# Kernel tuning notes

Measured on AMD Instinct MI355X. Metric: run time of the kernel, lower is better.

Reference implementation:

```python
import jax, jax.numpy as jnp
import numpy as np

B, S, D_MODEL, H_DIM = 8, 4096, 512, 120  # h = 1, so d_k = h_dim = 120
NEG_INF = jnp.float32(-1e9)
L2_EPS = 1e-12  # F.normalize eps


def setup_inputs() -> dict:
    key = jax.random.key(0)
    k_q, k_m, k_w, k_wt = jax.random.split(key, 4)
    query = jax.random.normal(k_q, (B, S, D_MODEL), dtype=jnp.float32)
    mask = jax.random.randint(k_m, (B, S, S), 0, 2, dtype=jnp.int32)
    # q_linear params (kaiming-uniform-ish init scale)
    lim = 1.0 / np.sqrt(D_MODEL)
    w_q = jax.random.uniform(k_w, (H_DIM, D_MODEL), jnp.float32, -lim, lim)
    b_q = jnp.zeros((H_DIM,), jnp.float32)
    # weight_tensor: shape (h, d_k) = (1, 120), xavier-uniform scale
    wt_lim = np.sqrt(6.0 / (1 + H_DIM))
    weight_tensor = jax.random.uniform(k_wt, (1, H_DIM), jnp.float32, -wt_lim, wt_lim)
    return {"query": query, "mask": mask, "w_q": w_q, "b_q": b_q,
            "weight_tensor": weight_tensor}


def reference(query, mask, w_q, b_q, weight_tensor):
    # context = q_linear(query).view(B, -1, h_dim); with h=1 the view is identity
    context = jnp.einsum("bsd,kd->bsk", query, w_q) + b_q          # [B, S, 120]
    # weighted then L2-normalized (cosine-similarity) features
    ctx = context * weight_tensor[:, None, :]                        # bcast (1,1,120)
    norm = jnp.sqrt(jnp.sum(ctx * ctx, axis=-1, keepdims=True))
    ctx_n = ctx / jnp.maximum(norm, L2_EPS)
    scores = jnp.einsum("bqk,bpk->bqp", ctx_n, ctx_n)               # [B, S, S]
    scores = jnp.where(mask == 0, NEG_INF, scores)                   # masked_fill
    return jax.nn.softmax(scores, axis=-1)                           # dropout: eval/identity
```

## Files before the change

### kernel.cpp

```cpp
#include <hip/hip_runtime.h>
#include <hip/hip_bf16.h>
#include <stdint.h>

#define BATCH 8
#define SEQ   4096
#define DM    512
#define HD    120

typedef __bf16   v8bf  __attribute__((ext_vector_type(8)));
typedef float    v4f   __attribute__((ext_vector_type(4)));
typedef int      i4    __attribute__((ext_vector_type(4)));
typedef uint32_t u32x2 __attribute__((ext_vector_type(2)));
typedef uint32_t u32x4 __attribute__((ext_vector_type(4)));
typedef float    f32x4 __attribute__((ext_vector_type(4)));

static __device__ __forceinline__ ushort f2bf(float x) {
  uint32_t u = __builtin_bit_cast(uint32_t, x);
  return (ushort)((u + 0x7fffu + ((u >> 16) & 1u)) >> 16);
}

static __device__ __forceinline__ void gld16(const void* g, void* l) {
  __builtin_amdgcn_global_load_lds(
      (const __attribute__((address_space(1))) uint32_t*)g,
      (__attribute__((address_space(3))) uint32_t*)l, 16, 0, 0);
}

__global__ __launch_bounds__(256) void ctx_kernel(
    const float* __restrict__ q, const float* __restrict__ wq,
    const float* __restrict__ bq, const float* __restrict__ wt,
    ushort* __restrict__ ctx)
{
  __shared__ __align__(16) float qs[32][68];
  __shared__ __align__(16) float ws2[32][136];

  const int t  = threadIdx.x;
  const int tx = t & 31, ty = t >> 5;
  const size_t row0 = (size_t)blockIdx.x * 64;
  const int qr = t >> 2, qk = (t & 3) * 8;

  float acc[8][4];
  #pragma unroll
  for (int j = 0; j < 8; ++j)
    #pragma unroll
    for (int i = 0; i < 4; ++i) acc[j][i] = 0.f;

  for (int k0 = 0; k0 < DM; k0 += 32) {
    __syncthreads();
    {
      f32x4 v0 = *(const f32x4*)&q[(row0 + qr) * DM + k0 + qk];
      f32x4 v1 = *(const f32x4*)&q[(row0 + qr) * DM + k0 + qk + 4];
      #pragma unroll
      for (int i = 0; i < 4; ++i) qs[qk + i][qr] = v0[i];
      #pragma unroll
      for (int i = 0; i < 4; ++i) qs[qk + 4 + i][qr] = v1[i];
    }
    #pragma unroll
    for (int i = 0; i < 16; ++i) {
      int flat = t + i * 256;
      int kk = flat & 31, c = flat >> 5;
      ws2[kk][c] = (c < HD) ? wq[c * DM + k0 + kk] : 0.f;
    }
    __syncthreads();
    #pragma unroll
    for (int kk = 0; kk < 32; ++kk) {
      f32x4 bv = *(const f32x4*)&ws2[kk][tx * 4];
      f32x4 a0 = *(const f32x4*)&qs[kk][ty * 8];
      f32x4 a1 = *(const f32x4*)&qs[kk][ty * 8 + 4];
      #pragma unroll
      for (int r = 0; r < 4; ++r)
        #pragma unroll
        for (int c = 0; c < 4; ++c) {
          acc[r][c]     = fmaf(a0[r], bv[c], acc[r][c]);
          acc[4 + r][c] = fmaf(a1[r], bv[c], acc[4 + r][c]);
        }
    }
  }

  float wtv[4], bqv[4];
  #pragma unroll
  for (int i = 0; i < 4; ++i) {
    int c = tx * 4 + i;
    wtv[i] = (c < HD) ? wt[c] : 0.f;
    bqv[i] = (c < HD) ? bq[c] : 0.f;
  }
  #pragma unroll
  for (int j = 0; j < 8; ++j) {
    int r = ty * 8 + j;
    float v[4]; float ss = 0.f;
    #pragma unroll
    for (int i = 0; i < 4; ++i) {
      v[i] = (acc[j][i] + bqv[i]) * wtv[i];
      ss = fmaf(v[i], v[i], ss);
    }
    #pragma unroll
    for (int xm = 1; xm < 32; xm <<= 1) ss += __shfl_xor(ss, xm, 64);
    float rinv = 1.f / fmaxf(sqrtf(ss), 1e-12f);
    uint32_t p0 = (uint32_t)f2bf(v[0] * rinv) | ((uint32_t)f2bf(v[1] * rinv) << 16);
    uint32_t p1 = (uint32_t)f2bf(v[2] * rinv) | ((uint32_t)f2bf(v[3] * rinv) << 16);
    u32x2 o = {p0, p1};
    char* dst = (char*)ctx + (row0 + r) * 256 +
                (((tx >> 1) * 16) ^ ((r & 7) << 4)) + (tx & 1) * 8;
    *(u32x2*)dst = o;
  }
}

#define MFMA(A, B, C) __builtin_amdgcn_mfma_f32_16x16x32_bf16(A, B, C, 0, 0, 0)

static __device__ __forceinline__ v8bf ldfrag(const char* base, int row, int slot) {
  int byte = row * 256 + ((slot * 16) ^ ((row & 7) << 4));
  return __builtin_bit_cast(v8bf, *(const u32x4*)(base + byte));
}

#define STAGE(buf, j) do {                                                    \
  const char* _gs = ctxb + (size_t)(j) * 64 * 256;                            \
  _Pragma("unroll")                                                           \
  for (int _i = 0; _i < 4; ++_i)                                              \
    gld16(_gs + (w * 4 + _i) * 1024 + lane * 16, (buf) + (w * 4 + _i) * 1024);\
} while (0)

#define LDM(dst, j) do {                                                      \
  _Pragma("unroll")                                                           \
  for (int _t = 0; _t < 4; ++_t)                                              \
    dst[_t] = *(const i4*)(mrow + (size_t)(j) * 64 + _t * 16 + g * 4);        \
} while (0)

#define QKT(buf, acc) do {                                                    \
  _Pragma("unroll")                                                           \
  for (int _t = 0; _t < 4; ++_t) {                                            \
    acc[_t] = (v4f){0.f, 0.f, 0.f, 0.f};                                      \
    _Pragma("unroll")                                                         \
    for (int _k = 0; _k < 4; ++_k) {                                          \
      v8bf _a = ldfrag(buf, _t * 16 + ln, _k * 4 + g);                        \
      acc[_t] = MFMA(_a, qf[_k], acc[_t]);                                    \
    }                                                                         \
  }                                                                           \
} while (0)

__global__ __launch_bounds__(256) void attn_kernel(
    const ushort* __restrict__ ctx, const int* __restrict__ mask,
    uint32_t* __restrict__ wsbits, float* __restrict__ out)
{
  __shared__ __align__(16) char lds[32768];
  char* B0 = lds;
  char* B1 = lds + 16384;

  const int t    = threadIdx.x;
  const int b    = blockIdx.x & 7;
  const int tile = blockIdx.x >> 3;
  const int w    = t >> 6, lane = t & 63;
  const int ln   = lane & 15, g = lane >> 4;
  const int qrow = tile * 64 + w * 16 + ln;
  const char* ctxb = (const char*)ctx + (size_t)b * SEQ * 256;
  const int*  __restrict__ mrow = mask + ((size_t)b * SEQ + qrow) * SEQ;
  float*      __restrict__ orow = out + ((size_t)b * SEQ + qrow) * SEQ;
  uint32_t*   __restrict__ wsb  = wsbits + ((size_t)blockIdx.x * 4 + w) * 2048;

  v8bf qf[4];
  #pragma unroll
  for (int kk = 0; kk < 4; ++kk) {
    int slot = kk * 4 + g;
    qf[kk] = *(const v8bf*)(ctxb + (size_t)qrow * 256 +
                            ((slot * 16) ^ ((qrow & 7) << 4)));
  }

  float lsum = 0.f;
  uint32_t lob = 0;
  i4 mc[4], mn[4];

  STAGE(B0, 0);
  LDM(mc, 0);
  __syncthreads();

  for (int j = 0; j < 64; ++j) {
    char* cur = (j & 1) ? B1 : B0;
    char* nxt = (j & 1) ? B0 : B1;
    if (j < 63) { STAGE(nxt, j + 1); LDM(mn, j + 1); }

    v4f acc[4];
    QKT(cur, acc);

    uint32_t tb = 0;
    #pragma unroll
    for (int t2 = 0; t2 < 4; ++t2)
      #pragma unroll
      for (int i = 0; i < 4; ++i) {
        float e = __expf(acc[t2][i] - 1.0f);
        lsum += mc[t2][i] ? e : 0.f;
        tb |= (uint32_t)(mc[t2][i] != 0) << (t2 * 4 + i);
      }
    if (j & 1) wsb[(j >> 1) * 64 + lane] = lob | (tb << 16);
    else       lob = tb;

    if (j < 63) {
      #pragma unroll
      for (int t2 = 0; t2 < 4; ++t2) mc[t2] = mn[t2];
    }
    __syncthreads();
  }

  lsum += __shfl_xor(lsum, 16, 64);
  lsum += __shfl_xor(lsum, 32, 64);
  const float lir = (lsum > 0.f) ? (1.f / lsum) : 0.f;

  asm volatile("s_waitcnt vmcnt(0)" ::: "memory");

  uint32_t bcur = wsb[lane];
  uint32_t bnxt = 0;
  STAGE(B0, 0);
  __syncthreads();

  for (int j = 0; j < 64; ++j) {
    char* cur = (j & 1) ? B1 : B0;
    char* nxt = (j & 1) ? B0 : B1;
    if (j < 63) STAGE(nxt, j + 1);
    if (!(j & 1) && j < 62) bnxt = wsb[((j >> 1) + 1) * 64 + lane];

    v4f acc[4];
    QKT(cur, acc);

    uint32_t bb = bcur >> ((j & 1) * 16);
    #pragma unroll
    for (int t2 = 0; t2 < 4; ++t2) {
      f32x4 o;
      #pragma unroll
      for (int i = 0; i < 4; ++i)
        o[i] = ((bb >> (t2 * 4 + i)) & 1u) ? __expf(acc[t2][i] - 1.0f) * lir : 0.f;
      *(f32x4*)(orow + (size_t)j * 64 + t2 * 16 + g * 4) = o;
    }
    if (j & 1) bcur = bnxt;
    __syncthreads();
  }
}

extern "C" void kernel_launch(void* const* d_in, const int* in_sizes, int n_in,
                              void* d_out, int out_size, void* d_ws, size_t ws_size,
                              hipStream_t stream) {
  const float* query = (const float*)d_in[0];
  const int*   mask  = (const int*)d_in[1];
  const float* w_q   = (const float*)d_in[2];
  const float* b_q   = (const float*)d_in[3];
  const float* wt    = (const float*)d_in[4];
  float* out = (float*)d_out;

  ushort*   ctx    = (ushort*)d_ws;
  uint32_t* wsbits = (uint32_t*)((char*)d_ws + (16u << 20));

  ctx_kernel<<<dim3(BATCH * SEQ / 64), dim3(256), 0, stream>>>(query, w_q, b_q, wt, ctx);
  attn_kernel<<<dim3(512), dim3(256), 0, stream>>>(ctx, mask, wsbits, out);
}
```

Measured before the change: 438.3 us.

## Pack mask to bits in prep kernel and stage ctx via registers

```diff
diff --git a/kernel.cpp b/kernel.cpp
--- a/kernel.cpp
+++ b/kernel.cpp
@@ -19,23 +19,43 @@
   return (ushort)((u + 0x7fffu + ((u >> 16) & 1u)) >> 16);
 }
 
-static __device__ __forceinline__ void gld16(const void* g, void* l) {
-  __builtin_amdgcn_global_load_lds(
-      (const __attribute__((address_space(1))) uint32_t*)g,
-      (__attribute__((address_space(3))) uint32_t*)l, 16, 0, 0);
-}
-
-__global__ __launch_bounds__(256) void ctx_kernel(
+__global__ __launch_bounds__(256) void prep_kernel(
     const float* __restrict__ q, const float* __restrict__ wq,
     const float* __restrict__ bq, const float* __restrict__ wt,
-    ushort* __restrict__ ctx)
+    const int* __restrict__ mask, ushort* __restrict__ ctx,
+    uint32_t* __restrict__ bits)
 {
   __shared__ __align__(16) float qs[32][68];
   __shared__ __align__(16) float ws2[32][136];
 
-  const int t  = threadIdx.x;
+  const int t = threadIdx.x;
+  const int cb = blockIdx.x >> 1;
+
+  if (blockIdx.x & 1) {
+    const size_t row0 = (size_t)cb * 64;
+    const int rhalf = t >> 7;
+    const int pw    = t & 127;
+    const int* mbase = mask + row0 * SEQ;
+    uint32_t* bbase  = bits + row0 * 128;
+    for (int s = 0; s < 32; ++s) {
+      int row = s * 2 + rhalf;
+      const int* mp = mbase + (size_t)row * SEQ + pw * 32;
+      uint32_t wd = 0;
+      #pragma unroll
+      for (int k = 0; k < 8; ++k) {
+        i4 m = *(const i4*)(mp + k * 4);
+        wd |= (uint32_t)(m.x != 0) << (k * 4);
+        wd |= (uint32_t)(m.y != 0) << (k * 4 + 1);
+        wd |= (uint32_t)(m.z != 0) << (k * 4 + 2);
+        wd |= (uint32_t)(m.w != 0) << (k * 4 + 3);
+      }
+      bbase[(size_t)row * 128 + pw] = wd;
+    }
+    return;
+  }
+
   const int tx = t & 31, ty = t >> 5;
-  const size_t row0 = (size_t)blockIdx.x * 64;
+  const size_t row0 = (size_t)cb * 64;
   const int qr = t >> 2, qk = (t & 3) * 8;
 
   float acc[8][4];
@@ -111,17 +131,16 @@
   return __builtin_bit_cast(v8bf, *(const u32x4*)(base + byte));
 }
 
-#define STAGE(buf, j) do {                                                    \
-  const char* _gs = ctxb + (size_t)(j) * 64 * 256;                            \
-  _Pragma("unroll")                                                           \
-  for (int _i = 0; _i < 4; ++_i)                                              \
-    gld16(_gs + (w * 4 + _i) * 1024 + lane * 16, (buf) + (w * 4 + _i) * 1024);\
-} while (0)
-
-#define LDM(dst, j) do {                                                      \
-  _Pragma("unroll")                                                           \
-  for (int _t = 0; _t < 4; ++_t)                                              \
-    dst[_t] = *(const i4*)(mrow + (size_t)(j) * 64 + _t * 16 + g * 4);        \
+#define STG_LOAD(R, j) do {                                                   \
+  const char* _g = ctxb + (size_t)(j) * 16384 + w * 4096 + lane * 16;         \
+  R##0 = *(const u32x4*)(_g);        R##1 = *(const u32x4*)(_g + 1024);       \
+  R##2 = *(const u32x4*)(_g + 2048); R##3 = *(const u32x4*)(_g + 3072);       \
+} while (0)
+
+#define STG_WRITE(R, buf) do {                                                \
+  char* _l = (buf) + w * 4096 + lane * 16;                                    \
+  *(u32x4*)(_l)        = R##0;  *(u32x4*)(_l + 1024) = R##1;                  \
+  *(u32x4*)(_l + 2048) = R##2;  *(u32x4*)(_l + 3072) = R##3;                  \
 } while (0)
 
 #define QKT(buf, acc) do {                                                    \
@@ -136,9 +155,39 @@
   }                                                                           \
 } while (0)
 
+#define EPIA(BW) do {                                                         \
+  _Pragma("unroll")                                                           \
+  for (int _t2 = 0; _t2 < 4; ++_t2) {                                         \
+    uint32_t nib = ((_t2 < 2 ? (BW).x : (BW).y) >> ((_t2 & 1) * 16 + g * 4)); \
+    _Pragma("unroll")                                                         \
+    for (int _i = 0; _i < 4; ++_i) {                                          \
+      float e = __expf(acc[_t2][_i] - 1.0f);                                  \
+      lsum += ((nib >> _i) & 1u) ? e : 0.f;                                   \
+    }                                                                         \
+  }                                                                           \
+} while (0)
+
+#define EPIB(BW, j) do {                                                      \
+  _Pragma("unroll")                                                           \
+  for (int _t2 = 0; _t2 < 4; ++_t2) {                                         \
+    uint32_t nib = ((_t2 < 2 ? (BW).x : (BW).y) >> ((_t2 & 1) * 16 + g * 4)); \
+    f32x4 o;                                                                  \
+    _Pragma("unroll")                                                         \
+    for (int _i = 0; _i < 4; ++_i)                                            \
+      o[_i] = ((nib >> _i) & 1u) ? __expf(acc[_t2][_i] - 1.0f) * lir : 0.f;   \
+    *(f32x4*)(orow + (size_t)(j) * 64 + _t2 * 16 + g * 4) = o;                \
+  }                                                                           \
+} while (0)
+
+#define BAR() do {                                                            \
+  asm volatile("s_waitcnt lgkmcnt(0)" ::: "memory");                          \
+  __builtin_amdgcn_s_barrier();                                               \
+  __builtin_amdgcn_sched_barrier(0);                                          \
+} while (0)
+
 __global__ __launch_bounds__(256) void attn_kernel(
-    const ushort* __restrict__ ctx, const int* __restrict__ mask,
-    uint32_t* __restrict__ wsbits, float* __restrict__ out)
+    const ushort* __restrict__ ctx, const uint32_t* __restrict__ bits,
+    float* __restrict__ out)
 {
   __shared__ __align__(16) char lds[32768];
   char* B0 = lds;
@@ -151,9 +200,8 @@
   const int ln   = lane & 15, g = lane >> 4;
   const int qrow = tile * 64 + w * 16 + ln;
   const char* ctxb = (const char*)ctx + (size_t)b * SEQ * 256;
-  const int*  __restrict__ mrow = mask + ((size_t)b * SEQ + qrow) * SEQ;
-  float*      __restrict__ orow = out + ((size_t)b * SEQ + qrow) * SEQ;
-  uint32_t*   __restrict__ wsb  = wsbits + ((size_t)blockIdx.x * 4 + w) * 2048;
+  const uint32_t* __restrict__ brow = bits + ((size_t)b * SEQ + qrow) * 128;
+  float*          __restrict__ orow = out + ((size_t)b * SEQ + qrow) * SEQ;
 
   v8bf qf[4];
   #pragma unroll
@@ -163,72 +211,58 @@
                             ((slot * 16) ^ ((qrow & 7) << 4)));
   }
 
+  u32x4 sA0, sA1, sA2, sA3, sB0, sB1, sB2, sB3;
+  u32x2 bw0 = {0, 0}, bw1 = {0, 0}, bwn0 = {0, 0}, bwn1 = {0, 0};
   float lsum = 0.f;
-  uint32_t lob = 0;
-  i4 mc[4], mn[4];
-
-  STAGE(B0, 0);
-  LDM(mc, 0);
+
+  STG_LOAD(sA, 0);
+  bw0 = *(const u32x2*)(brow);
+  bw1 = *(const u32x2*)(brow + 2);
+  STG_WRITE(sA, B0);
+  STG_LOAD(sB, 1);
   __syncthreads();
 
-  for (int j = 0; j < 64; ++j) {
-    char* cur = (j & 1) ? B1 : B0;
-    char* nxt = (j & 1) ? B0 : B1;
-    if (j < 63) { STAGE(nxt, j + 1); LDM(mn, j + 1); }
-
+  for (int jj = 0; jj < 64; jj += 2) {
     v4f acc[4];
-    QKT(cur, acc);
-
-    uint32_t tb = 0;
-    #pragma unroll
-    for (int t2 = 0; t2 < 4; ++t2)
-      #pragma unroll
-      for (int i = 0; i < 4; ++i) {
-        float e = __expf(acc[t2][i] - 1.0f);
-        lsum += mc[t2][i] ? e : 0.f;
-        tb |= (uint32_t)(mc[t2][i] != 0) << (t2 * 4 + i);
-      }
-    if (j & 1) wsb[(j >> 1) * 64 + lane] = lob | (tb << 16);
-    else       lob = tb;
-
-    if (j < 63) {
-      #pragma unroll
-      for (int t2 = 0; t2 < 4; ++t2) mc[t2] = mn[t2];
-    }
-    __syncthreads();
+    if (jj + 2 < 64) { STG_LOAD(sA, jj + 2); bwn0 = *(const u32x2*)(brow + (jj + 2) * 2); }
+    QKT(B0, acc);
+    STG_WRITE(sB, B1);
+    EPIA(bw0);
+    BAR();
+
+    if (jj + 3 < 64) { STG_LOAD(sB, jj + 3); bwn1 = *(const u32x2*)(brow + (jj + 3) * 2); }
+    QKT(B1, acc);
+    if (jj + 2 < 64) STG_WRITE(sA, B0);
+    EPIA(bw1);
+    bw0 = bwn0; bw1 = bwn1;
+    BAR();
   }
 
   lsum += __shfl_xor(lsum, 16, 64);
   lsum += __shfl_xor(lsum, 32, 64);
   const float lir = (lsum > 0.f) ? (1.f / lsum) : 0.f;
 
-  asm volatile("s_waitcnt vmcnt(0)" ::: "memory");
-
-  uint32_t bcur = wsb[lane];
-  uint32_t bnxt = 0;
-  STAGE(B0, 0);
+  STG_LOAD(sA, 0);
+  bw0 = *(const u32x2*)(brow);
+  bw1 = *(const u32x2*)(brow + 2);
+  STG_WRITE(sA, B0);
+  STG_LOAD(sB, 1);
   __syncthreads();
 
-  for (int j = 0; j < 64; ++j) {
-    char* cur = (j & 1) ? B1 : B0;
-    char* nxt = (j & 1) ? B0 : B1;
-    if (j < 63) STAGE(nxt, j + 1);
-    if (!(j & 1) && j < 62) bnxt = wsb[((j >> 1) + 1) * 64 + lane];
-
+  for (int jj = 0; jj < 64; jj += 2) {
     v4f acc[4];
-    QKT(cur, acc);
-
-    uint32_t bb = bcur >> ((j & 1) * 16);
-    #pragma unroll
-    for (int t2 = 0; t2 < 4; ++t2) {
-      f32x4 o;
-      #pragma unroll
-      for (int i = 0; i < 4; ++i)
-        o[i] = ((bb >> (t2 * 4 + i)) & 1u) ? __expf(acc[t2][i] - 1.0f) * lir : 0.f;
-      *(f32x4*)(orow + (size_t)j * 64 + t2 * 16 + g * 4) = o;
-    }
-    if (j & 1) bcur = bnxt;
-    __syncthreads();
+    if (jj + 2 < 64) { STG_LOAD(sA, jj + 2); bwn0 = *(const u32x2*)(brow + (jj + 2) * 2); }
+    QKT(B0, acc);
+    STG_WRITE(sB, B1);
+    EPIB(bw0, jj);
+    BAR();
+
+    if (jj + 3 < 64) { STG_LOAD(sB, jj + 3); bwn1 = *(const u32x2*)(brow + (jj + 3) * 2); }
+    QKT(B1, acc);
+    if (jj + 2 < 64) STG_WRITE(sA, B0);
+    EPIB(bw1, jj + 1);
+    bw0 = bwn0; bw1 = bwn1;
+    BAR();
   }
 }
 
@@ -242,9 +276,9 @@
   const float* wt    = (const float*)d_in[4];
   float* out = (float*)d_out;
 
-  ushort*   ctx    = (ushort*)d_ws;
-  uint32_t* wsbits = (uint32_t*)((char*)d_ws + (16u << 20));
-
-  ctx_kernel<<<dim3(BATCH * SEQ / 64), dim3(256), 0, stream>>>(query, w_q, b_q, wt, ctx);
-  attn_kernel<<<dim3(512), dim3(256), 0, stream>>>(ctx, mask, wsbits, out);
-}
+  ushort*   ctx  = (ushort*)d_ws;
+  uint32_t* bits = (uint32_t*)((char*)d_ws + (16u << 20));
+
+  prep_kernel<<<dim3(1024), dim3(256), 0, stream>>>(query, w_q, b_q, wt, mask, ctx, bits);
+  attn_kernel<<<dim3(512), dim3(256), 0, stream>>>(ctx, bits, out);
+}
```

After: 395.7 us. -9.7%, faster.
